# Optimization experiments

Hardware: AMD Instinct MI355X
Metric: run time of the kernel (lower is better)

## Reference

```python
import jax, jax.numpy as jnp
import numpy as np

HIDDEN = 256
NUM_REL = 6
NUM_BASES = 30
N_NODES = 50000
N_EDGES = 800000


def rgcn_gate_layer(x, src, dst, etype, basis, att, root, bias, gate_w, gate_b):
    # Basis-decomposed relation weights: W_r = sum_b att[r,b] * basis[b]
    N = x.shape[0]
    W = jnp.einsum('rb,bio->rio', att, basis)           # [R, d, d]
    # Transform all nodes under every relation (cheaper than per-edge matmul
    # since N*R < E), then gather the per-edge message.
    xw = jnp.einsum('nd,rde->rne', x, W)                # [R, N, d]
    msg = xw[etype, src]                                # [E, d]
    # Scalar sigmoid gate per edge message
    g = jax.nn.sigmoid(msg @ gate_w + gate_b)           # [E, 1]
    gated = g * msg
    # Mean aggregation over incoming edges per destination node
    agg = jax.ops.segment_sum(gated, dst, num_segments=N)
    deg = jax.ops.segment_sum(jnp.ones((src.shape[0], 1), x.dtype), dst,
                              num_segments=N)
    agg = agg / jnp.maximum(deg, 1.0)
    return agg + x @ root + bias


def setup_inputs() -> dict:
    key = jax.random.key(0)
    ks = jax.random.split(key, 16)
    d = HIDDEN
    inp = {
        'x': jax.random.normal(ks[0], (N_NODES, d), jnp.float32),
        'edge_src': jax.random.randint(ks[1], (N_EDGES,), 0, N_NODES, jnp.int32),
        'edge_dst': jax.random.randint(ks[2], (N_EDGES,), 0, N_NODES, jnp.int32),
        'edge_type': jax.random.randint(ks[3], (N_EDGES,), 0, NUM_REL, jnp.int32),
    }
    def glorot(k, shape):
        fan = shape[-2] + shape[-1]
        return jax.random.uniform(k, shape, jnp.float32,
                                  -np.sqrt(6.0 / fan), np.sqrt(6.0 / fan))
    for li, off in ((1, 4), (2, 10)):
        inp[f'basis{li}'] = glorot(ks[off + 0], (NUM_BASES, d, d))
        inp[f'att{li}'] = glorot(ks[off + 1], (NUM_REL, NUM_BASES))
        inp[f'root{li}'] = glorot(ks[off + 2], (d, d))
        inp[f'bias{li}'] = jnp.zeros((d,), jnp.float32)
        inp[f'gate_w{li}'] = glorot(ks[off + 3], (d, 1))
        inp[f'gate_b{li}'] = jnp.zeros((1,), jnp.float32)
    return inp


def reference(x, edge_src, edge_dst, edge_type,
              basis1, att1, root1, bias1, gate_w1, gate_b1,
              basis2, att2, root2, bias2, gate_w2, gate_b2):
    h = jax.nn.relu(rgcn_gate_layer(x, edge_src, edge_dst, edge_type,
                                    basis1, att1, root1, bias1,
                                    gate_w1, gate_b1))
    out = rgcn_gate_layer(h, edge_src, edge_dst, edge_type,
                          basis2, att2, root2, bias2, gate_w2, gate_b2)
    return out
```

## Files before the change

### kernel.cpp

```cpp
#include <hip/hip_runtime.h>
#include <cmath>

#define HIDDEN 256
#define NUM_REL 6
#define KA 1536
#define KB 1792
#define NK 56
#define NKA 48
#define CTSTRIDE 28672

typedef float f32x4_t __attribute__((ext_vector_type(4)));
typedef short bf16x8_t __attribute__((ext_vector_type(8)));

__device__ __forceinline__ float bf2f(ushort u) {
  return __uint_as_float(((uint)u) << 16);
}
__device__ __forceinline__ ushort f2bf(float f) {
  uint u = __float_as_uint(f);
  u += 0x7FFFu + ((u >> 16) & 1u);
  return (ushort)(u >> 16);
}

__global__ __launch_bounds__(256) void prep_weights(
    const float* __restrict__ att, const float* __restrict__ basis,
    const float* __restrict__ root, const float* __restrict__ gw,
    ushort* __restrict__ BTf, float* __restrict__ gatevec) {
  const int d = blockIdx.x, r = blockIdx.y, o = threadIdx.x;
  float v;
  if (r < 6) {
    float s = 0.f;
#pragma unroll
    for (int b = 0; b < 30; ++b)
      s += att[r * 30 + b] * basis[(size_t)b * 65536 + d * 256 + o];
    v = s;
  } else {
    v = root[d * 256 + o];
  }
  const int gk = r * 256 + d;
  BTf[(size_t)(o >> 4) * CTSTRIDE + (gk >> 3) * 128 + (o & 15) * 8 +
      (gk & 7)] = f2bf(v);
  if (r < 6) {
    float t = v * gw[o];
#pragma unroll
    for (int off = 32; off; off >>= 1) t += __shfl_xor(t, off);
    __shared__ float sums[4];
    if ((o & 63) == 0) sums[o >> 6] = t;
    __syncthreads();
    if (o == 0) gatevec[r * 256 + d] = sums[0] + sums[1] + sums[2] + sums[3];
  }
}

__global__ __launch_bounds__(256) void gdot_kernel(
    const void* __restrict__ xin, int xIsF32, ushort* __restrict__ xbOut,
    const float* __restrict__ gatevec, const float* __restrict__ gate_b,
    float* __restrict__ G, int N) {
  const int wave = (blockIdx.x * blockDim.x + threadIdx.x) >> 6;
  if (wave >= N) return;
  const int l = threadIdx.x & 63;
  float x0, x1, x2, x3;
  if (xIsF32) {
    float4 xv = ((const float4*)xin)[(size_t)wave * 64 + l];
    x0 = xv.x; x1 = xv.y; x2 = xv.z; x3 = xv.w;
    ushort4 o;
    o.x = f2bf(x0); o.y = f2bf(x1); o.z = f2bf(x2); o.w = f2bf(x3);
    ((ushort4*)xbOut)[(size_t)wave * 64 + l] = o;
  } else {
    ushort4 xv = ((const ushort4*)xin)[(size_t)wave * 64 + l];
    x0 = bf2f(xv.x); x1 = bf2f(xv.y); x2 = bf2f(xv.z); x3 = bf2f(xv.w);
  }
  float out = 0.f;
#pragma unroll
  for (int r = 0; r < NUM_REL; ++r) {
    float4 gv = ((const float4*)(gatevec + r * 256))[l];
    float d = x0 * gv.x + x1 * gv.y + x2 * gv.z + x3 * gv.w;
#pragma unroll
    for (int off = 32; off; off >>= 1) d += __shfl_xor(d, off);
    if (l == r) out = d;
  }
  if (l < NUM_REL) {
    const float gb = gate_b[0];
    G[(size_t)l * N + wave] = 1.f / (1.f + __expf(-(out + gb)));
  }
}

#define ACCUM(rj, gj, vj)                                                  \
  do {                                                                    \
    const float fx = (gj)*bf2f((vj).x), fy = (gj)*bf2f((vj).y);           \
    const float fz = (gj)*bf2f((vj).z), fw = (gj)*bf2f((vj).w);           \
    switch (rj) {                                                         \
      case 0: a0x += fx; a0y += fy; a0z += fz; a0w += fw; break;          \
      case 1: a1x += fx; a1y += fy; a1z += fz; a1w += fw; break;          \
      case 2: a2x += fx; a2y += fy; a2z += fz; a2w += fw; break;          \
      case 3: a3x += fx; a3y += fy; a3z += fz; a3w += fw; break;          \
      case 4: a4x += fx; a4y += fy; a4z += fz; a4w += fw; break;          \
      default: a5x += fx; a5y += fy; a5z += fz; a5w += fw; break;         \
    }                                                                     \
  } while (0)

#define RELOF(ei) ((ei >= b1) + (ei >= b2) + (ei >= b3) + (ei >= b4) + (ei >= b5))

__global__ __launch_bounds__(256) void edge_agg(
    const ushort* __restrict__ xb, const float* __restrict__ G,
    const int* __restrict__ rp8, const int* __restrict__ src_s,
    ushort* __restrict__ A, int N) {
  const int n = (blockIdx.x * blockDim.x + threadIdx.x) >> 6;
  if (n >= N) return;
  const int l = threadIdx.x & 63;
  const int b0 = rp8[n * 8 + 0], b1 = rp8[n * 8 + 1], b2 = rp8[n * 8 + 2];
  const int b3 = rp8[n * 8 + 3], b4 = rp8[n * 8 + 4], b5 = rp8[n * 8 + 5];
  const int b6 = rp8[n * 8 + 6];

  float a0x = 0, a0y = 0, a0z = 0, a0w = 0, a1x = 0, a1y = 0, a1z = 0, a1w = 0;
  float a2x = 0, a2y = 0, a2z = 0, a2w = 0, a3x = 0, a3y = 0, a3z = 0, a3w = 0;
  float a4x = 0, a4y = 0, a4z = 0, a4w = 0, a5x = 0, a5y = 0, a5z = 0, a5w = 0;

  int e = b0;
  for (; e + 7 < b6; e += 8) {
    const int s0 = src_s[e + 0], s1 = src_s[e + 1];
    const int s2 = src_s[e + 2], s3 = src_s[e + 3];
    const int s4 = src_s[e + 4], s5 = src_s[e + 5];
    const int s6 = src_s[e + 6], s7 = src_s[e + 7];
    const ushort4 v0 = ((const ushort4*)(xb + (size_t)s0 * 256))[l];
    const ushort4 v1 = ((const ushort4*)(xb + (size_t)s1 * 256))[l];
    const ushort4 v2 = ((const ushort4*)(xb + (size_t)s2 * 256))[l];
    const ushort4 v3 = ((const ushort4*)(xb + (size_t)s3 * 256))[l];
    const ushort4 v4 = ((const ushort4*)(xb + (size_t)s4 * 256))[l];
    const ushort4 v5 = ((const ushort4*)(xb + (size_t)s5 * 256))[l];
    const ushort4 v6 = ((const ushort4*)(xb + (size_t)s6 * 256))[l];
    const ushort4 v7 = ((const ushort4*)(xb + (size_t)s7 * 256))[l];
    const int r0 = RELOF(e + 0), r1 = RELOF(e + 1), r2 = RELOF(e + 2),
              r3 = RELOF(e + 3), r4 = RELOF(e + 4), r5 = RELOF(e + 5),
              r6 = RELOF(e + 6), r7 = RELOF(e + 7);
    const float g0 = G[(size_t)r0 * N + s0], g1 = G[(size_t)r1 * N + s1];
    const float g2 = G[(size_t)r2 * N + s2], g3 = G[(size_t)r3 * N + s3];
    const float g4 = G[(size_t)r4 * N + s4], g5 = G[(size_t)r5 * N + s5];
    const float g6 = G[(size_t)r6 * N + s6], g7 = G[(size_t)r7 * N + s7];
    ACCUM(r0, g0, v0); ACCUM(r1, g1, v1); ACCUM(r2, g2, v2); ACCUM(r3, g3, v3);
    ACCUM(r4, g4, v4); ACCUM(r5, g5, v5); ACCUM(r6, g6, v6); ACCUM(r7, g7, v7);
  }
  for (; e < b6; ++e) {
    const int s0 = src_s[e];
    const ushort4 v0 = ((const ushort4*)(xb + (size_t)s0 * 256))[l];
    const int r0 = RELOF(e);
    const float g0 = G[(size_t)r0 * N + s0];
    ACCUM(r0, g0, v0);
  }

  const float inv = 1.f / fmaxf((float)(b6 - b0), 1.f);
  ushort* Arow = A + (size_t)n * KA;
  ushort4 o;
  o.x = f2bf(a0x * inv); o.y = f2bf(a0y * inv); o.z = f2bf(a0z * inv); o.w = f2bf(a0w * inv);
  ((ushort4*)(Arow + 0 * 256))[l] = o;
  o.x = f2bf(a1x * inv); o.y = f2bf(a1y * inv); o.z = f2bf(a1z * inv); o.w = f2bf(a1w * inv);
  ((ushort4*)(Arow + 1 * 256))[l] = o;
  o.x = f2bf(a2x * inv); o.y = f2bf(a2y * inv); o.z = f2bf(a2z * inv); o.w = f2bf(a2w * inv);
  ((ushort4*)(Arow + 2 * 256))[l] = o;
  o.x = f2bf(a3x * inv); o.y = f2bf(a3y * inv); o.z = f2bf(a3z * inv); o.w = f2bf(a3w * inv);
  ((ushort4*)(Arow + 3 * 256))[l] = o;
  o.x = f2bf(a4x * inv); o.y = f2bf(a4y * inv); o.z = f2bf(a4z * inv); o.w = f2bf(a4w * inv);
  ((ushort4*)(Arow + 4 * 256))[l] = o;
  o.x = f2bf(a5x * inv); o.y = f2bf(a5y * inv); o.z = f2bf(a5z * inv); o.w = f2bf(a5w * inv);
  ((ushort4*)(Arow + 5 * 256))[l] = o;
}

__global__ __launch_bounds__(256) void gemm_fused(
    const ushort* __restrict__ A, const ushort* __restrict__ xb,
    const ushort* __restrict__ BTf, const float* __restrict__ bias,
    void* __restrict__ outPtr, int M, int mode) {
  __shared__ ushort As[3][64 * 32];
  const int bid = blockIdx.x;
  const int row0 = (bid >> 1) * 64;
  const int colh = bid & 1;
  const int tid = threadIdx.x;
  const int w = tid >> 6, l = tid & 63;

  const int srow = tid >> 2;
  const int ssc = (tid & 3) ^ (srow & 3) ^ ((srow >> 2) & 3);
  const int ga = min(row0 + srow, M - 1);
  const ushort* gpA = A + (size_t)ga * KA + ssc * 8;
  const ushort* gpX = xb + (size_t)ga * 256 + ssc * 8;

  const ushort* Bb = BTf + (size_t)(colh * 8 + w * 2) * CTSTRIDE +
                     (l >> 4) * 128 + (l & 15) * 8;

  f32x4_t acc[4][2] = {};

  auto stage = [&](int k, int buf) {
    const ushort* gp = (k < NKA) ? (gpA + k * 32) : (gpX + (k * 32 - KA));
    __builtin_amdgcn_global_load_lds(
        (const __attribute__((address_space(1))) void*)gp,
        (__attribute__((address_space(3))) void*)(&As[buf][tid * 8]), 16, 0, 0);
  };

  auto compute = [&](int buf, const bf16x8_t* b) {
    bf16x8_t a[4];
#pragma unroll
    for (int m = 0; m < 4; ++m) {
      const int rr = m * 16 + (l & 15);
      const int c = (l >> 4) ^ (rr & 3) ^ ((rr >> 2) & 3);
      a[m] = *(const bf16x8_t*)(&As[buf][rr * 32 + c * 8]);
    }
#pragma unroll
    for (int m = 0; m < 4; ++m)
#pragma unroll
      for (int n = 0; n < 2; ++n)
        acc[m][n] = __builtin_amdgcn_mfma_f32_16x16x32_bf16(a[m], b[n],
                                                            acc[m][n], 0, 0, 0);
  };

  bf16x8_t bE[2], bO[2];
  stage(0, 0);
  stage(1, 1);
#pragma unroll
  for (int n = 0; n < 2; ++n)
    bE[n] = *(const bf16x8_t*)(Bb + (size_t)n * CTSTRIDE);

  for (int k = 0; k < NK; k += 2) {
    asm volatile("s_waitcnt vmcnt(3)" ::: "memory");
    __builtin_amdgcn_s_barrier();
#pragma unroll
    for (int n = 0; n < 2; ++n)
      bO[n] = *(const bf16x8_t*)(Bb + (size_t)n * CTSTRIDE + (k + 1) * 512);
    if (k + 2 < NK) stage(k + 2, (k + 2) % 3);
    compute(k % 3, bE);

    asm volatile("s_waitcnt vmcnt(3)" ::: "memory");
    __builtin_amdgcn_s_barrier();
    if (k + 2 < NK) {
#pragma unroll
      for (int n = 0; n < 2; ++n)
        bE[n] = *(const bf16x8_t*)(Bb + (size_t)n * CTSTRIDE + (k + 2) * 512);
    }
    if (k + 3 < NK) stage(k + 3, (k + 3) % 3);
    compute((k + 1) % 3, bO);
  }

  const int rbase = row0 + (l >> 4) * 4;
  const int cbase = colh * 128 + w * 32 + (l & 15);
#pragma unroll
  for (int n = 0; n < 2; ++n) {
    const int col = cbase + n * 16;
    const float bv = bias[col];
#pragma unroll
    for (int m = 0; m < 4; ++m)
#pragma unroll
      for (int i = 0; i < 4; ++i) {
        const int row = rbase + m * 16 + i;
        if (row < M) {
          float v = acc[m][n][i] + bv;
          if (mode == 0) {
            v = fmaxf(v, 0.f);
            ((ushort*)outPtr)[(size_t)row * 256 + col] = f2bf(v);
          } else {
            ((float*)outPtr)[(size_t)row * 256 + col] = v;
          }
        }
      }
  }
}

__global__ void hist_kernel(const int* __restrict__ dst,
                            const int* __restrict__ ety,
                            int* __restrict__ cnt, int* __restrict__ erank,
                            int E) {
  int stride = gridDim.x * blockDim.x;
  for (int e = blockIdx.x * blockDim.x + threadIdx.x; e < E; e += stride)
    erank[e] = atomicAdd(&cnt[dst[e] * 8 + ety[e]], 1);
}

__global__ void scan_reduce(const int* __restrict__ cnt,
                            int* __restrict__ blockSums, int n) {
  __shared__ int sd[256];
  int base = blockIdx.x * 1024;
  int t = threadIdx.x;
  int s = 0;
#pragma unroll
  for (int i = 0; i < 4; ++i) {
    int idx = base + t * 4 + i;
    s += (idx < n) ? cnt[idx] : 0;
  }
  sd[t] = s; __syncthreads();
  for (int off = 128; off; off >>= 1) {
    if (t < off) sd[t] += sd[t + off];
    __syncthreads();
  }
  if (t == 0) blockSums[blockIdx.x] = sd[0];
}

__global__ void scan_offsets(int* __restrict__ blockSums, int nb) {
  __shared__ int sd[512];
  const int t = threadIdx.x;
  const int v = (t < nb) ? blockSums[t] : 0;
  sd[t] = v; __syncthreads();
  for (int off = 1; off < 512; off <<= 1) {
    int u = (t >= off) ? sd[t - off] : 0;
    __syncthreads();
    sd[t] += u;
    __syncthreads();
  }
  if (t < nb) blockSums[t] = sd[t] - v;
}

__global__ void scan_write(const int* __restrict__ cnt,
                           const int* __restrict__ blockSums,
                           int* __restrict__ row_ptr, int n) {
  __shared__ int sd[256];
  int base = blockIdx.x * 1024;
  int t = threadIdx.x;
  int v[4]; int s = 0;
#pragma unroll
  for (int i = 0; i < 4; ++i) {
    int idx = base + t * 4 + i;
    v[i] = (idx < n) ? cnt[idx] : 0;
    s += v[i];
  }
  sd[t] = s; __syncthreads();
  for (int off = 1; off < 256; off <<= 1) {
    int val = (t >= off) ? sd[t - off] : 0;
    __syncthreads();
    sd[t] += val;
    __syncthreads();
  }
  int excl = blockSums[blockIdx.x] + sd[t] - s;
  for (int i = 0; i < 4; ++i) {
    int idx = base + t * 4 + i;
    if (idx < n) {
      row_ptr[idx] = excl;
      excl += v[i];
      if (idx == n - 1) row_ptr[n] = excl;
    }
  }
}

__global__ void scatter_kernel(const int* __restrict__ src,
                               const int* __restrict__ dst,
                               const int* __restrict__ ety,
                               const int* __restrict__ row_ptr,
                               const int* __restrict__ erank,
                               int* __restrict__ src_s, int E) {
  int stride = gridDim.x * blockDim.x;
  for (int e = blockIdx.x * blockDim.x + threadIdx.x; e < E; e += stride) {
    int bin = dst[e] * 8 + ety[e];
    src_s[row_ptr[bin] + erank[e]] = src[e];
  }
}

static inline size_t align16(size_t x) { return (x + 15) & ~(size_t)15; }

extern "C" void kernel_launch(void* const* d_in, const int* in_sizes, int n_in,
                              void* d_out, int out_size, void* d_ws,
                              size_t ws_size, hipStream_t stream) {
  const float* x    = (const float*)d_in[0];
  const int*   src  = (const int*)d_in[1];
  const int*   dst  = (const int*)d_in[2];
  const int*   ety  = (const int*)d_in[3];

  const int N   = in_sizes[0] / HIDDEN;
  const int E   = in_sizes[1];
  const int RN2 = N * 8;

  char* p = (char*)d_ws;
  ushort* BTf    = (ushort*)p; p += align16(((size_t)16 * CTSTRIDE + 4096) * 2);
  float* gatevec = (float*)p;  p += align16((size_t)NUM_REL * 256 * 4);
  float* G       = (float*)p;  p += align16((size_t)NUM_REL * N * 4);
  ushort* xb0    = (ushort*)p; p += align16((size_t)N * HIDDEN * 2);
  ushort* xb1    = (ushort*)p; p += align16((size_t)N * HIDDEN * 2);
  int* cnt       = (int*)p;    p += align16((size_t)RN2 * 4);
  int* erank     = (int*)p;    p += align16((size_t)E * 4);
  int* row_ptr   = (int*)p;    p += align16((size_t)(RN2 + 1) * 4);
  int* blockSums = (int*)p;    p += 2048;
  int* src_s     = (int*)p;    p += align16((size_t)E * 4);
  ushort* A      = (ushort*)p;

  const int scanBlocks = (RN2 + 1023) / 1024;

  hipMemsetAsync(cnt, 0, (size_t)RN2 * sizeof(int), stream);
  hist_kernel<<<2048, 256, 0, stream>>>(dst, ety, cnt, erank, E);
  scan_reduce<<<scanBlocks, 256, 0, stream>>>(cnt, blockSums, RN2);
  scan_offsets<<<1, 512, 0, stream>>>(blockSums, scanBlocks);
  scan_write<<<scanBlocks, 256, 0, stream>>>(cnt, blockSums, row_ptr, RN2);
  scatter_kernel<<<2048, 256, 0, stream>>>(src, dst, ety, row_ptr, erank,
                                           src_s, E);

  const int nodeBlocks = (N * 64 + 255) / 256;
  const int gemmGrid = 2 * ((N + 63) / 64);

  for (int layer = 0; layer < 2; ++layer) {
    const float* bas  = (const float*)d_in[layer ? 10 : 4];
    const float* att  = (const float*)d_in[layer ? 11 : 5];
    const float* root = (const float*)d_in[layer ? 12 : 6];
    const float* bias = (const float*)d_in[layer ? 13 : 7];
    const float* gw   = (const float*)d_in[layer ? 14 : 8];
    const float* gb   = (const float*)d_in[layer ? 15 : 9];
    const ushort* xb  = layer ? xb1 : xb0;
    void* outp = layer ? d_out : (void*)xb1;
    const int mode = layer ? 1 : 0;

    prep_weights<<<dim3(256, 7), 256, 0, stream>>>(att, bas, root, gw, BTf,
                                                   gatevec);
    gdot_kernel<<<nodeBlocks, 256, 0, stream>>>(
        layer ? (const void*)xb1 : (const void*)x, layer ? 0 : 1, xb0,
        gatevec, gb, G, N);
    edge_agg<<<nodeBlocks, 256, 0, stream>>>(xb, G, row_ptr, src_s, A, N);
    gemm_fused<<<gemmGrid, 256, 0, stream>>>(A, xb, BTf, bias, outp, N, mode);
  }
}
```

Before: 494.0 us.

## Widen GEMM tile to full 256 columns and deepen K step to 64

The fused GEMM now computes all 256 output columns per 64-row block instead of splitting columns across two blocks, so each A tile is loaded from global memory once rather than twice. The K step per pipeline stage doubles to 64, with a new 8-way XOR swizzle in shared memory and a larger per-wave accumulator (4x4 MFMA tiles). This halves the grid size and raises register and LDS use per block, which may lower occupancy and reduce the number of blocks available to fill the GPU.

```diff
diff --git a/kernel.cpp b/kernel.cpp
--- a/kernel.cpp
+++ b/kernel.cpp
@@ -5,8 +5,8 @@
 #define NUM_REL 6
 #define KA 1536
 #define KB 1792
-#define NK 56
-#define NKA 48
+#define NK64 28
+#define NKA64 24
 #define CTSTRIDE 28672
 
 typedef float f32x4_t __attribute__((ext_vector_type(4)));
@@ -167,78 +167,97 @@
     const ushort* __restrict__ A, const ushort* __restrict__ xb,
     const ushort* __restrict__ BTf, const float* __restrict__ bias,
     void* __restrict__ outPtr, int M, int mode) {
-  __shared__ ushort As[3][64 * 32];
-  const int bid = blockIdx.x;
-  const int row0 = (bid >> 1) * 64;
-  const int colh = bid & 1;
+  __shared__ ushort As[3][64 * 64];
+  const int row0 = blockIdx.x * 64;
   const int tid = threadIdx.x;
   const int w = tid >> 6, l = tid & 63;
 
-  const int srow = tid >> 2;
-  const int ssc = (tid & 3) ^ (srow & 3) ^ ((srow >> 2) & 3);
-  const int ga = min(row0 + srow, M - 1);
-  const ushort* gpA = A + (size_t)ga * KA + ssc * 8;
-  const ushort* gpX = xb + (size_t)ga * 256 + ssc * 8;
-
-  const ushort* Bb = BTf + (size_t)(colh * 8 + w * 2) * CTSTRIDE +
-                     (l >> 4) * 128 + (l & 15) * 8;
-
-  f32x4_t acc[4][2] = {};
+  const int srow0 = tid >> 3;
+  const int gc = (tid & 7) ^ (srow0 & 7);
+  const int ga0 = min(row0 + srow0, M - 1);
+  const int ga1 = min(row0 + 32 + srow0, M - 1);
+  const ushort* gpA0 = A + (size_t)ga0 * KA + gc * 8;
+  const ushort* gpA1 = A + (size_t)ga1 * KA + gc * 8;
+  const ushort* gpX0 = xb + (size_t)ga0 * 256 + gc * 8;
+  const ushort* gpX1 = xb + (size_t)ga1 * 256 + gc * 8;
+
+  const ushort* Bb =
+      BTf + (size_t)(w * 4) * CTSTRIDE + (l >> 4) * 128 + (l & 15) * 8;
+
+  f32x4_t acc[4][4] = {};
 
   auto stage = [&](int k, int buf) {
-    const ushort* gp = (k < NKA) ? (gpA + k * 32) : (gpX + (k * 32 - KA));
+    const int ko = k * 64;
+    const ushort* g0 = (k < NKA64) ? (gpA0 + ko) : (gpX0 + (ko - KA));
+    const ushort* g1 = (k < NKA64) ? (gpA1 + ko) : (gpX1 + (ko - KA));
     __builtin_amdgcn_global_load_lds(
-        (const __attribute__((address_space(1))) void*)gp,
-        (__attribute__((address_space(3))) void*)(&As[buf][tid * 8]), 16, 0, 0);
+        (const __attribute__((address_space(1))) void*)g0,
+        (__attribute__((address_space(3))) void*)(&As[buf][(size_t)tid * 8]),
+        16, 0, 0);
+    __builtin_amdgcn_global_load_lds(
+        (const __attribute__((address_space(1))) void*)g1,
+        (__attribute__((address_space(3))) void*)(&As[buf][(size_t)(256 + tid) * 8]),
+        16, 0, 0);
   };
 
-  auto compute = [&](int buf, const bf16x8_t* b) {
-    bf16x8_t a[4];
-#pragma unroll
-    for (int m = 0; m < 4; ++m) {
-      const int rr = m * 16 + (l & 15);
-      const int c = (l >> 4) ^ (rr & 3) ^ ((rr >> 2) & 3);
-      a[m] = *(const bf16x8_t*)(&As[buf][rr * 32 + c * 8]);
+  auto compute = [&](int buf, const bf16x8_t (*b)[4]) {
+#pragma unroll
+    for (int ks = 0; ks < 2; ++ks) {
+      bf16x8_t a[4];
+#pragma unroll
+      for (int m = 0; m < 4; ++m) {
+        const int rr = m * 16 + (l & 15);
+        const int s = (ks * 4 + (l >> 4)) ^ (rr & 7);
+        a[m] = *(const bf16x8_t*)(&As[buf][rr * 64 + s * 8]);
+      }
+#pragma unroll
+      for (int m = 0; m < 4; ++m)
+#pragma unroll
+        for (int n = 0; n < 4; ++n)
+          acc[m][n] = __builtin_amdgcn_mfma_f32_16x16x32_bf16(
+              a[m], b[ks][n], acc[m][n], 0, 0, 0);
     }
-#pragma unroll
-    for (int m = 0; m < 4; ++m)
-#pragma unroll
-      for (int n = 0; n < 2; ++n)
-        acc[m][n] = __builtin_amdgcn_mfma_f32_16x16x32_bf16(a[m], b[n],
-                                                            acc[m][n], 0, 0, 0);
   };
 
-  bf16x8_t bE[2], bO[2];
+  bf16x8_t bE[2][4], bO[2][4];
   stage(0, 0);
   stage(1, 1);
 #pragma unroll
-  for (int n = 0; n < 2; ++n)
-    bE[n] = *(const bf16x8_t*)(Bb + (size_t)n * CTSTRIDE);
-
-  for (int k = 0; k < NK; k += 2) {
-    asm volatile("s_waitcnt vmcnt(3)" ::: "memory");
+  for (int ks = 0; ks < 2; ++ks)
+#pragma unroll
+    for (int n = 0; n < 4; ++n)
+      bE[ks][n] = *(const bf16x8_t*)(Bb + (size_t)n * CTSTRIDE + ks * 512);
+
+  for (int k = 0; k < NK64; k += 2) {
+    asm volatile("s_waitcnt vmcnt(10)" ::: "memory");
     __builtin_amdgcn_s_barrier();
 #pragma unroll
-    for (int n = 0; n < 2; ++n)
-      bO[n] = *(const bf16x8_t*)(Bb + (size_t)n * CTSTRIDE + (k + 1) * 512);
-    if (k + 2 < NK) stage(k + 2, (k + 2) % 3);
+    for (int ks = 0; ks < 2; ++ks)
+#pragma unroll
+      for (int n = 0; n < 4; ++n)
+        bO[ks][n] = *(const bf16x8_t*)(Bb + (size_t)n * CTSTRIDE +
+                                       (size_t)(k + 1) * 1024 + ks * 512);
+    if (k + 2 < NK64) stage(k + 2, (k + 2) % 3);
     compute(k % 3, bE);
 
-    asm volatile("s_waitcnt vmcnt(3)" ::: "memory");
+    asm volatile("s_waitcnt vmcnt(10)" ::: "memory");
     __builtin_amdgcn_s_barrier();
-    if (k + 2 < NK) {
-#pragma unroll
-      for (int n = 0; n < 2; ++n)
-        bE[n] = *(const bf16x8_t*)(Bb + (size_t)n * CTSTRIDE + (k + 2) * 512);
+    if (k + 2 < NK64) {
+#pragma unroll
+      for (int ks = 0; ks < 2; ++ks)
+#pragma unroll
+        for (int n = 0; n < 4; ++n)
+          bE[ks][n] = *(const bf16x8_t*)(Bb + (size_t)n * CTSTRIDE +
+                                         (size_t)(k + 2) * 1024 + ks * 512);
     }
-    if (k + 3 < NK) stage(k + 3, (k + 3) % 3);
+    if (k + 3 < NK64) stage(k + 3, (k + 3) % 3);
     compute((k + 1) % 3, bO);
   }
 
   const int rbase = row0 + (l >> 4) * 4;
-  const int cbase = colh * 128 + w * 32 + (l & 15);
-#pragma unroll
-  for (int n = 0; n < 2; ++n) {
+  const int cbase = w * 64 + (l & 15);
+#pragma unroll
+  for (int n = 0; n < 4; ++n) {
     const int col = cbase + n * 16;
     const float bv = bias[col];
 #pragma unroll
@@ -383,7 +402,7 @@
                                            src_s, E);
 
   const int nodeBlocks = (N * 64 + 255) / 256;
-  const int gemmGrid = 2 * ((N + 63) / 64);
+  const int gemmGrid = (N + 63) / 64;
 
   for (int layer = 0; layer < 2; ++layer) {
     const float* bas  = (const float*)d_in[layer ? 10 : 4];
```

New measurement: 482.7 us, median of 2. 2.3% less time.
